# Performance work log

Measured on AMD Instinct MI355X. Metric: run time of the kernel, lower is better.

## Reference

```python
import jax, jax.numpy as jnp
import numpy as np

B, C, H, W = 8, 3, 1024, 1024
N, D, PS, NB, NH = 512, 256, 16, 8, 4


def _bin_matrix():
    # static radial-binning averaging matrix for a PS x (PS//2+1) rfft2 spectrum
    h, w = PS, PS // 2 + 1
    fy = np.fft.fftfreq(h)
    fx = np.linspace(0.0, 0.5, w)
    r = np.sqrt(fx[None, :] ** 2 + fy[:, None] ** 2)
    max_r = r.max() + 1e-6
    edges = np.linspace(0.0, max_r, NB + 1)
    idx = np.clip(np.searchsorted(edges, r.ravel(), side='right') - 1, 0, NB - 1)
    M = np.zeros((NB, h * w), np.float32)
    M[idx, np.arange(h * w)] = 1.0
    cnt = M.sum(1, keepdims=True)
    return M / np.maximum(cnt, 1.0)

_BIN_M = jnp.asarray(_bin_matrix())


def _ln(x, g, b, eps=1e-5):
    m = x.mean(-1, keepdims=True)
    v = x.var(-1, keepdims=True)
    return g * (x - m) / jnp.sqrt(v + eps) + b


def _gelu(x):
    return jax.nn.gelu(x, approximate=False)


def setup_inputs() -> dict:
    key = jax.random.key(0)
    ks = jax.random.split(key, 16)
    xav = lambda k, o, i: (jax.random.normal(k, (o, i)) / np.sqrt(i)).astype(jnp.float32)
    z = lambda n: jnp.zeros((n,), jnp.float32)
    o1 = lambda n: jnp.ones((n,), jnp.float32)
    FD = 2 * NB
    return {
        'image': jax.random.normal(ks[0], (B, C, H, W), jnp.float32),
        'point_coords': jax.random.uniform(ks[1], (B, N, 2), jnp.float32, 0.0, float(W)),
        'point_labels': jax.random.randint(ks[2], (B, N), 0, 2),
        'pe_w': xav(ks[3], D, D), 'pe_b': z(D),
        'type_emb': (0.02 * jax.random.normal(ks[4], (2, D))).astype(jnp.float32),
        'fbi': (1.0 + 0.1 * jax.random.normal(ks[5], (NB,))).astype(jnp.float32),
        'fe1_w': xav(ks[6], D // 2, FD), 'fe1_b': z(D // 2),
        'feln1_g': o1(D // 2), 'feln1_b': z(D // 2),
        'fe2_w': xav(ks[7], D, D // 2), 'fe2_b': z(D),
        'feln2_g': o1(D), 'feln2_b': z(D),
        'in_w': xav(ks[8], 3 * D, D), 'in_b': z(3 * D),
        'ao_w': xav(ks[9], D, D), 'ao_b': z(D),
        'n1_g': o1(D), 'n1_b': z(D),
        'f1_w': xav(ks[10], 2 * D, D), 'f1_b': z(2 * D),
        'f2_w': xav(ks[11], D, 2 * D), 'f2_b': z(D),
        'n2_g': o1(D), 'n2_b': z(D),
        'op_w': xav(ks[12], D, D), 'op_b': z(D),
    }


def reference(image, point_coords, point_labels, pe_w, pe_b, type_emb, fbi,
              fe1_w, fe1_b, feln1_g, feln1_b, fe2_w, fe2_b, feln2_g, feln2_b,
              in_w, in_b, ao_w, ao_b, n1_g, n1_b, f1_w, f1_b, f2_w, f2_b,
              n2_g, n2_b, op_w, op_b):
    Bv, Cv, Hv, Wv = image.shape
    Nv = point_coords.shape[1]
    # --- sinusoidal positional encoding (SAM style) + linear proj ---
    nc = point_coords / jnp.array([Wv, Hv], jnp.float32)
    dim_t = 10000.0 ** (2.0 * jnp.arange(D // 4, dtype=jnp.float32) / (D // 4))
    ax = (nc[..., 0:1] * (2.0 * np.pi)) / dim_t          # [B,N,D/4]
    ay = (nc[..., 1:2] * (2.0 * np.pi)) / dim_t
    pe = jnp.concatenate([jnp.sin(ax), jnp.cos(ax), jnp.sin(ay), jnp.cos(ay)], -1)
    spatial = pe @ pe_w.T + pe_b + type_emb[point_labels]  # [B,N,D]
    # --- batched per-point patch gather + rfft2 + radial binning ---
    gray = image.mean(1)                                   # [B,H,W]
    pc = jax.lax.stop_gradient(point_coords)               # .long() detaches in torch
    half = PS // 2
    px = jnp.clip(pc[..., 0].astype(jnp.int32), half, Wv - half - 1)
    py = jnp.clip(pc[..., 1].astype(jnp.int32), half, Hv - half - 1)
    off = jnp.arange(PS) - half
    rows = py[..., None] + off                             # [B,N,PS]
    cols = px[..., None] + off
    bidx = jnp.arange(Bv)[:, None, None, None]
    patches = gray[bidx, rows[..., :, None], cols[..., None, :]]  # [B,N,PS,PS]
    fft = jnp.fft.rfft2(patches, norm='ortho')             # [B,N,PS,PS//2+1]
    mag_bins = jnp.abs(fft).reshape(Bv, Nv, -1) @ _BIN_M.T    # [B,N,NB]
    ph_bins = jnp.angle(fft).reshape(Bv, Nv, -1) @ _BIN_M.T
    feat = jnp.concatenate([mag_bins * jax.nn.softmax(fbi), ph_bins], -1)  # [B,N,2*NB]
    # --- freq encoder MLP ---
    h1 = _gelu(_ln(feat @ fe1_w.T + fe1_b, feln1_g, feln1_b))
    freq = _ln(h1 @ fe2_w.T + fe2_b, feln2_g, feln2_b)     # [B,N,D]
    # --- cross-attention fusion (spatial = Q, freq = K/V) ---
    hd = D // NH
    q = (spatial @ in_w[:D].T + in_b[:D]).reshape(Bv, Nv, NH, hd)
    k = (freq @ in_w[D:2 * D].T + in_b[D:2 * D]).reshape(Bv, Nv, NH, hd)
    v = (freq @ in_w[2 * D:].T + in_b[2 * D:]).reshape(Bv, Nv, NH, hd)
    att = jax.nn.softmax(jnp.einsum('bqhd,bkhd->bhqk', q, k) / np.sqrt(hd), -1)
    o = jnp.einsum('bhqk,bkhd->bqhd', att, v).reshape(Bv, Nv, D)
    x = _ln(spatial + (o @ ao_w.T + ao_b), n1_g, n1_b)
    ffn = _gelu(x @ f1_w.T + f1_b) @ f2_w.T + f2_b
    x = _ln(x + ffn, n2_g, n2_b)
    return x @ op_w.T + op_b
```

## Files before the change

### kernel.cpp

```cpp
#include <hip/hip_runtime.h>
#include <math.h>


typedef __attribute__((ext_vector_type(8))) short short8;
typedef __attribute__((ext_vector_type(4))) float floatx4;
typedef unsigned short u16;
typedef unsigned long long u64;

__device__ __forceinline__ float gelu_f(float x) {
  return 0.5f * x * (1.0f + erff(x * 0.70710678118654752f));
}

__device__ __forceinline__ u16 bf16_rn(float x) {
  union { float f; unsigned u; } v; v.f = x;
  unsigned r = v.u + 0x7fffu + ((v.u >> 16) & 1u);
  return (u16)(r >> 16);
}

__device__ __forceinline__ void split_bf16(float x, u16& h, u16& l) {
  h = bf16_rn(x);
  union { unsigned u; float f; } hv; hv.u = ((unsigned)h) << 16;
  l = bf16_rn(x - hv.f);
}

__device__ __forceinline__ float join_bf16(u16 h, u16 l) {
  union { unsigned u; float f; } a, b;
  a.u = ((unsigned)h) << 16;
  b.u = ((unsigned)l) << 16;
  return a.f + b.f;
}

#define W_PE   0
#define W_FE1  65536
#define W_FE2  67584
#define W_IN   100352
#define W_AO   296960
#define W_F1   362496
#define W_F2   493568
#define W_OP   624640


template <int NA, int K>
__device__ __forceinline__ void mm16_swz(
    const u16* Ah, const u16* Al, const int S,
    const u16* __restrict__ Bh, const u16* __restrict__ Bl,
    floatx4* acc)
{
  const int t = threadIdx.x;
  const int w = t >> 6, lane = t & 63;
  const int lm = lane & 15, kg = lane >> 4;
  #pragma unroll
  for (int it = 0; it < K / 32; ++it) {
    const short8 a_h = *(const short8*)&Ah[lm * S + it * 32 + kg * 8];
    const short8 a_l = *(const short8*)&Al[lm * S + it * 32 + kg * 8];
    #pragma unroll
    for (int nj = 0; nj < NA; nj++) {
      const size_t wo = (size_t)(((w * NA + nj) * (K / 32) + it) * 512 + lane * 8);
      const short8 b_h = *(const short8*)&Bh[wo];
      const short8 b_l = *(const short8*)&Bl[wo];
      acc[nj] = __builtin_amdgcn_mfma_f32_16x16x32_bf16(a_h, b_h, acc[nj], 0, 0, 0);
      acc[nj] = __builtin_amdgcn_mfma_f32_16x16x32_bf16(a_h, b_l, acc[nj], 0, 0, 0);
      acc[nj] = __builtin_amdgcn_mfma_f32_16x16x32_bf16(a_l, b_h, acc[nj], 0, 0, 0);
    }
  }
}

template <int NA, int K, int NSETS>
__device__ __forceinline__ void mm16_ks(
    const u16* Ah, const u16* Al, const int S,
    const u16* __restrict__ Bh, const u16* __restrict__ Bl,
    floatx4* acc)
{
  const int t = threadIdx.x;
  const int w = t >> 6, lane = t & 63;
  const int ww = w & 3, set = w >> 2;
  const int lm = lane & 15, kg = lane >> 4;
  constexpr int ITERS = K / (32 * NSETS);
  #pragma unroll
  for (int itl = 0; itl < ITERS; ++itl) {
    const int it = set * ITERS + itl;
    const short8 a_h = *(const short8*)&Ah[lm * S + it * 32 + kg * 8];
    const short8 a_l = *(const short8*)&Al[lm * S + it * 32 + kg * 8];
    #pragma unroll
    for (int nj = 0; nj < NA; nj++) {
      const size_t wo = (size_t)(((ww * NA + nj) * (K / 32) + it) * 512 + lane * 8);
      const short8 b_h = *(const short8*)&Bh[wo];
      const short8 b_l = *(const short8*)&Bl[wo];
      acc[nj] = __builtin_amdgcn_mfma_f32_16x16x32_bf16(a_h, b_h, acc[nj], 0, 0, 0);
      acc[nj] = __builtin_amdgcn_mfma_f32_16x16x32_bf16(a_h, b_l, acc[nj], 0, 0, 0);
      acc[nj] = __builtin_amdgcn_mfma_f32_16x16x32_bf16(a_l, b_h, acc[nj], 0, 0, 0);
    }
  }
}

template <int NA>
__device__ __forceinline__ void reduce_sets(floatx4* acc, float* PART)
{
  const int t = threadIdx.x;
  const int w = t >> 6, lane = t & 63;
  const int ww = w & 3, set = w >> 2;
  const int lm = lane & 15, kg = lane >> 4;
  __syncthreads();
  if (set != 0) {
    #pragma unroll
    for (int nj = 0; nj < NA; nj++) {
      const int col = ww * (NA * 16) + nj * 16 + lm;
      #pragma unroll
      for (int r = 0; r < 4; r++)
        PART[((set - 1) * 16 + kg * 4 + r) * 260 + col] = acc[nj][r];
    }
  }
  __syncthreads();
  if (set == 0) {
    #pragma unroll
    for (int nj = 0; nj < NA; nj++) {
      const int col = ww * (NA * 16) + nj * 16 + lm;
      #pragma unroll
      for (int r = 0; r < 4; r++) {
        const int rr = kg * 4 + r;
        acc[nj][r] += PART[rr * 260 + col] + PART[(16 + rr) * 260 + col]
                    + PART[(32 + rr) * 260 + col];
      }
    }
  }
}

__device__ __forceinline__ void stage16(
    const u16* __restrict__ Gh, const u16* __restrict__ Gl,
    u16* Lh, u16* Ll)
{
  const int t = threadIdx.x;
  #pragma unroll
  for (int i = 0; i < 2; i++) {
    const int s = t + i * 256;
    const int row = s >> 5, c = (s & 31) * 8;
    *(short8*)&Lh[row * 264 + c] = *(const short8*)&Gh[(size_t)row * 256 + c];
    *(short8*)&Ll[row * 264 + c] = *(const short8*)&Gl[(size_t)row * 256 + c];
  }
  __syncthreads();
}

template <int N_, int NA>
__device__ __forceinline__ void ln_rows(const float (&v)[NA][4], float* red1, float* red2,
                                        float (&mean)[4], float (&rstd)[4])
{
  const int t = threadIdx.x;
  const int w = t >> 6;
  const int lane = t & 63;
  const int kg = lane >> 4;
  float s1[4] = {0.f,0.f,0.f,0.f}, s2[4] = {0.f,0.f,0.f,0.f};
  #pragma unroll
  for (int nj = 0; nj < NA; nj++)
    #pragma unroll
    for (int r = 0; r < 4; r++) { s1[r] += v[nj][r]; s2[r] += v[nj][r] * v[nj][r]; }
  #pragma unroll
  for (int r = 0; r < 4; r++) {
    #pragma unroll
    for (int off = 1; off < 16; off <<= 1) {
      s1[r] += __shfl_xor(s1[r], off);
      s2[r] += __shfl_xor(s2[r], off);
    }
  }
  __syncthreads();
  if ((lane & 15) == 0) {
    #pragma unroll
    for (int r = 0; r < 4; r++) {
      red1[w * 16 + kg * 4 + r] = s1[r];
      red2[w * 16 + kg * 4 + r] = s2[r];
    }
  }
  __syncthreads();
  #pragma unroll
  for (int r = 0; r < 4; r++) {
    const int rw = kg * 4 + r;
    const float a = red1[rw] + red1[16 + rw] + red1[32 + rw] + red1[48 + rw];
    const float b = red2[rw] + red2[16 + rw] + red2[32 + rw] + red2[48 + rw];
    mean[r] = a * (1.0f / N_);
    rstd[r] = rsqrtf(b * (1.0f / N_) - mean[r] * mean[r] + 1e-5f);
  }
}

template <int N_, int NA>
__device__ __forceinline__ void ln_rows16(const float (&v)[NA][4], float* red1, float* red2,
                                          float (&mean)[4], float (&rstd)[4])
{
  const int t = threadIdx.x;
  const int w = t >> 6;
  const int lane = t & 63;
  const int ww = w & 3, set = w >> 2;
  const int kg = lane >> 4;
  float s1[4] = {0.f,0.f,0.f,0.f}, s2[4] = {0.f,0.f,0.f,0.f};
  #pragma unroll
  for (int nj = 0; nj < NA; nj++)
    #pragma unroll
    for (int r = 0; r < 4; r++) { s1[r] += v[nj][r]; s2[r] += v[nj][r] * v[nj][r]; }
  #pragma unroll
  for (int r = 0; r < 4; r++) {
    #pragma unroll
    for (int off = 1; off < 16; off <<= 1) {
      s1[r] += __shfl_xor(s1[r], off);
      s2[r] += __shfl_xor(s2[r], off);
    }
  }
  __syncthreads();
  if (set == 0 && (lane & 15) == 0) {
    #pragma unroll
    for (int r = 0; r < 4; r++) {
      red1[ww * 16 + kg * 4 + r] = s1[r];
      red2[ww * 16 + kg * 4 + r] = s2[r];
    }
  }
  __syncthreads();
  if (set == 0) {
    #pragma unroll
    for (int r = 0; r < 4; r++) {
      const int rw = kg * 4 + r;
      const float a = red1[rw] + red1[16 + rw] + red1[32 + rw] + red1[48 + rw];
      const float b = red2[rw] + red2[16 + rw] + red2[32 + rw] + red2[48 + rw];
      mean[r] = a * (1.0f / N_);
      rstd[r] = rsqrtf(b * (1.0f / N_) - mean[r] * mean[r] + 1e-5f);
    }
  }
}

__device__ __forceinline__ void store_swz(
    u16* __restrict__ Wh, u16* __restrict__ Wl, const int segbase,
    const int rel, const int kshift, const float4 v)
{
  const int K = 1 << kshift;
  const int n = rel >> kshift;
  const int k = rel & (K - 1);
  const int off8 = ((n >> 4) * (K >> 5) + (k >> 5)) * 512
                 + (((k >> 3) & 3) * 16 + (n & 15)) * 8 + (k & 7);
  u16 h0,h1,h2,h3,l0,l1,l2,l3;
  split_bf16(v.x,h0,l0); split_bf16(v.y,h1,l1);
  split_bf16(v.z,h2,l2); split_bf16(v.w,h3,l3);
  *(u64*)&Wh[segbase + off8] = (u64)h0 | ((u64)h1<<16) | ((u64)h2<<32) | ((u64)h3<<48);
  *(u64*)&Wl[segbase + off8] = (u64)l0 | ((u64)l1<<16) | ((u64)l2<<32) | ((u64)l3<<48);
}

__global__ __launch_bounds__(64) void k0_prep(
    const float* __restrict__ image, const float* __restrict__ coords,
    const float* __restrict__ fbi,
    const float* __restrict__ pe_w, const float* __restrict__ fe1_w,
    const float* __restrict__ fe2_w, const float* __restrict__ in_w,
    const float* __restrict__ ao_w, const float* __restrict__ f1_w,
    const float* __restrict__ f2_w, const float* __restrict__ op_w,
    u16* __restrict__ Wh, u16* __restrict__ Wl,
    u16* __restrict__ PEh, u16* __restrict__ PEl,
    u16* __restrict__ FEATh, u16* __restrict__ FEATl)
{
  const int blk = blockIdx.x;
  const int lane = threadIdx.x;

  if (blk < 2696) {
    const int idx = (blk * 64 + lane) * 4;
    if (idx < W_FE1) {
      store_swz(Wh, Wl, W_PE, idx - W_PE, 8, *(const float4*)&pe_w[idx - W_PE]);
    } else if (idx < W_FE2) {
      const int rel = idx - W_FE1;
      const float4 v = *(const float4*)&fe1_w[rel];
      u16 h0,h1,h2,h3,l0,l1,l2,l3;
      split_bf16(v.x,h0,l0); split_bf16(v.y,h1,l1);
      split_bf16(v.z,h2,l2); split_bf16(v.w,h3,l3);
      *(u64*)&Wh[idx] = (u64)h0 | ((u64)h1<<16) | ((u64)h2<<32) | ((u64)h3<<48);
      *(u64*)&Wl[idx] = (u64)l0 | ((u64)l1<<16) | ((u64)l2<<32) | ((u64)l3<<48);
    } else if (idx < W_IN) {
      store_swz(Wh, Wl, W_FE2, idx - W_FE2, 7, *(const float4*)&fe2_w[idx - W_FE2]);
    } else if (idx < W_AO) {
      store_swz(Wh, Wl, W_IN, idx - W_IN, 8, *(const float4*)&in_w[idx - W_IN]);
    } else if (idx < W_F1) {
      store_swz(Wh, Wl, W_AO, idx - W_AO, 8, *(const float4*)&ao_w[idx - W_AO]);
    } else if (idx < W_F2) {
      store_swz(Wh, Wl, W_F1, idx - W_F1, 8, *(const float4*)&f1_w[idx - W_F1]);
    } else if (idx < W_OP) {
      store_swz(Wh, Wl, W_F2, idx - W_F2, 9, *(const float4*)&f2_w[idx - W_F2]);
    } else {
      store_swz(Wh, Wl, W_OP, idx - W_OP, 8, *(const float4*)&op_w[idx - W_OP]);
    }
    return;
  }

  const int id = blk - 2696;
  const int b  = id >> 9;
  const float pcx = coords[id * 2 + 0];
  const float pcy = coords[id * 2 + 1];

  {
    const float TWO_PI = 6.283185307179586f;
    const float dimt = expf((float)lane * 0.28782313662425572f);
    const float ax = (pcx * (1.0f / 1024.0f)) * TWO_PI / dimt;
    const float ay = (pcy * (1.0f / 1024.0f)) * TWO_PI / dimt;
    u16 h, l;
    split_bf16(sinf(ax), h, l); PEh[id*256+lane]     = h; PEl[id*256+lane]     = l;
    split_bf16(cosf(ax), h, l); PEh[id*256+lane+64]  = h; PEl[id*256+lane+64]  = l;
    split_bf16(sinf(ay), h, l); PEh[id*256+lane+128] = h; PEl[id*256+lane+128] = l;
    split_bf16(cosf(ay), h, l); PEh[id*256+lane+192] = h; PEl[id*256+lane+192] = l;
  }

  int px = (int)pcx; px = px < 8 ? 8 : (px > 1015 ? 1015 : px);
  int py = (int)pcy; py = py < 8 ? 8 : (py > 1015 ? 1015 : py);

  __shared__ float patch[256];
  __shared__ float ct[16], st[16];
  __shared__ float Gre[144], Gim[144];
  __shared__ float msum[8], psum[8];
  __shared__ int cnt8[8];
  {
    const float* img = image + (size_t)b * 3145728;
    #pragma unroll
    for (int i = 0; i < 4; i++) {
      const int p = i * 64 + lane;
      const int r = p >> 4, c = p & 15;
      const int off = (py - 8 + r) * 1024 + (px - 8 + c);
      const float s = img[off] + img[off + 1048576] + img[off + 2097152];
      patch[r * 16 + c] = s * (1.0f / 3.0f);
    }
  }
  if (lane < 16) {
    float c, s;
    if ((lane & 3) == 0) {
      const float cv[4] = {1.0f, 0.0f, -1.0f, 0.0f};
      const float sv[4] = {0.0f, -1.0f, 0.0f, 1.0f};
      c = cv[lane >> 2]; s = sv[lane >> 2];
    } else {
      const float a = -3.14159265358979f * (float)lane * 0.125f;
      c = cosf(a); s = sinf(a);
    }
    ct[lane] = c; st[lane] = s;
  }
  if (lane < 8) { msum[lane] = 0.0f; psum[lane] = 0.0f; cnt8[lane] = 0; }
  __syncthreads();

  for (int tt = lane; tt < 144; tt += 64) {
    const int y = tt / 9, kx = tt - y * 9;
    float re = 0.0f, im = 0.0f;
    #pragma unroll
    for (int x = 0; x < 16; x++) {
      const int w = (x * kx) & 15;
      const float pv = patch[y * 16 + x];
      re = fmaf(pv, ct[w], re);
      im = fmaf(pv, st[w], im);
    }
    Gre[tt] = re; Gim[tt] = im;
  }
  __syncthreads();

  for (int tt = lane; tt < 144; tt += 64) {
    const int ky = tt / 9, kx = tt - ky * 9;
    float re = 0.0f, im = 0.0f;
    #pragma unroll
    for (int y = 0; y < 16; y++) {
      const int w = (y * ky) & 15;
      const float gr = Gre[y * 9 + kx], gi = Gim[y * 9 + kx];
      re = fmaf(gr, ct[w], re);
      re = fmaf(-gi, st[w], re);
      im = fmaf(gr, st[w], im);
      im = fmaf(gi, ct[w], im);
    }
    if (((ky & 7) == 0) && ((kx & 7) == 0)) im = 0.0f;
    const float mag = sqrtf(re * re + im * im) * 0.0625f;
    const float ph  = atan2f(im, re);

    const float fy = (ky < 8) ? (float)ky * 0.0625f : (float)(ky - 16) * 0.0625f;
    const float fx = (float)kx * 0.0625f;
    const float r = sqrtf(fx * fx + fy * fy);
    const float max_r = 0.7071077811865476f;
    const float stepf = max_r * 0.125f;
    int idx = 0;
    #pragma unroll
    for (int kq = 1; kq <= 8; kq++) {
      const float e = (kq == 8) ? max_r : stepf * (float)kq;
      if (r >= e) idx = kq;
    }
    if (idx > 7) idx = 7;
    atomicAdd(&msum[idx], mag);
    atomicAdd(&psum[idx], ph);
    atomicAdd(&cnt8[idx], 1);
  }
  __syncthreads();

  if (lane < 8) {
    float fm = fbi[0];
    #pragma unroll
    for (int j = 1; j < 8; j++) fm = fmaxf(fm, fbi[j]);
    float se = 0.0f;
    #pragma unroll
    for (int j = 0; j < 8; j++) se += expf(fbi[j] - fm);
    const float smx = expf(fbi[lane] - fm) / se;
    const float c = (float)(cnt8[lane] > 0 ? cnt8[lane] : 1);
    u16 h, l;
    split_bf16((msum[lane] / c) * smx, h, l);
    FEATh[id*16+lane] = h; FEATl[id*16+lane] = l;
    split_bf16(psum[lane] / c, h, l);
    FEATh[id*16+8+lane] = h; FEATl[id*16+8+lane] = l;
  }
}

__global__ __launch_bounds__(256) void k1_front(
    const u16* __restrict__ Wh, const u16* __restrict__ Wl,
    const u16* __restrict__ PEh, const u16* __restrict__ PEl,
    const u16* __restrict__ FEATh, const u16* __restrict__ FEATl,
    const float* __restrict__ pe_b, const int* __restrict__ labels,
    const float* __restrict__ temb,
    const float* __restrict__ fe1_b, const float* __restrict__ feln1_g, const float* __restrict__ feln1_b,
    const float* __restrict__ fe2_b, const float* __restrict__ feln2_g, const float* __restrict__ feln2_b,
    const float* __restrict__ in_b,
    u16* __restrict__ SPh, u16* __restrict__ SPl,
    u16* __restrict__ Qh, u16* __restrict__ Ql,
    u16* __restrict__ Kh, u16* __restrict__ Kl,
    u16* __restrict__ Vth, u16* __restrict__ Vtl)
{
  __shared__ __align__(16) u16 smem[12800];
  __shared__ float redbuf[128];
  const int blk = blockIdx.x;
  const int t = threadIdx.x;
  const int w = t >> 6, lane = t & 63;
  const int lm = lane & 15, kg = lane >> 4;

  if (blk < 256) {
    const int m0 = blk * 16;
    u16* Lh = smem;
    u16* Ll = smem + 4224;
    stage16(PEh + (size_t)m0 * 256, PEl + (size_t)m0 * 256, Lh, Ll);
    floatx4 acc[4];
    #pragma unroll
    for (int j = 0; j < 4; j++) acc[j] = (floatx4){0.f,0.f,0.f,0.f};
    mm16_swz<4, 256>(Lh, Ll, 264, Wh + W_PE, Wl + W_PE, acc);
    __syncthreads();
    #pragma unroll
    for (int nj = 0; nj < 4; nj++) {
      const int col = w * 64 + nj * 16 + lm;
      #pragma unroll
      for (int r = 0; r < 4; r++) {
        const int row = m0 + kg * 4 + r;
        const float v = acc[nj][r] + pe_b[col] + temb[labels[row] * 256 + col];
        u16 h, l; split_bf16(v, h, l);
        SPh[(size_t)row * 256 + col] = h;
        SPl[(size_t)row * 256 + col] = l;
        Lh[(kg * 4 + r) * 264 + col] = h;
        Ll[(kg * 4 + r) * 264 + col] = l;
      }
    }
    __syncthreads();

    floatx4 accq[4];
    #pragma unroll
    for (int j = 0; j < 4; j++) accq[j] = (floatx4){0.f,0.f,0.f,0.f};
    mm16_swz<4, 256>(Lh, Ll, 264, Wh + W_IN, Wl + W_IN, accq);
    #pragma unroll
    for (int nj = 0; nj < 4; nj++) {
      const int col = w * 64 + nj * 16 + lm;
      #pragma unroll
      for (int r = 0; r < 4; r++) {
        const int row = m0 + kg * 4 + r;
        u16 h, l; split_bf16(accq[nj][r] + in_b[col], h, l);
        Qh[(size_t)row * 256 + col] = h;
        Ql[(size_t)row * 256 + col] = l;
      }
    }
    return;
  }

  const int m0 = (blk - 256) * 16;
  u16* h1h = smem;
  u16* h1l = smem + 2176;
  u16* Ah  = smem + 4352;
  u16* Al  = smem + 8576;

  floatx4 acc1[2];
  acc1[0] = (floatx4){0.f,0.f,0.f,0.f};
  acc1[1] = (floatx4){0.f,0.f,0.f,0.f};
  {
    const short8 zz = {0,0,0,0,0,0,0,0};
    const short8 a_h = (kg < 2) ? *(const short8*)&FEATh[(size_t)(m0 + lm) * 16 + kg * 8] : zz;
    const short8 a_l = (kg < 2) ? *(const short8*)&FEATl[(size_t)(m0 + lm) * 16 + kg * 8] : zz;
    #pragma unroll
    for (int nj = 0; nj < 2; nj++) {
      const int col = w * 32 + nj * 16 + lm;
      const short8 b_h = (kg < 2) ? *(const short8*)&Wh[W_FE1 + (size_t)col * 16 + kg * 8] : zz;
      const short8 b_l = (kg < 2) ? *(const short8*)&Wl[W_FE1 + (size_t)col * 16 + kg * 8] : zz;
      acc1[nj] = __builtin_amdgcn_mfma_f32_16x16x32_bf16(a_h, b_h, acc1[nj], 0, 0, 0);
      acc1[nj] = __builtin_amdgcn_mfma_f32_16x16x32_bf16(a_h, b_l, acc1[nj], 0, 0, 0);
      acc1[nj] = __builtin_amdgcn_mfma_f32_16x16x32_bf16(a_l, b_h, acc1[nj], 0, 0, 0);
    }
  }

  float v1[2][4];
  #pragma unroll
  for (int nj = 0; nj < 2; nj++) {
    const int col = w * 32 + nj * 16 + lm;
    #pragma unroll
    for (int r = 0; r < 4; r++) v1[nj][r] = acc1[nj][r] + fe1_b[col];
  }
  float mean[4], rstd[4];
  ln_rows<128, 2>(v1, redbuf, redbuf + 64, mean, rstd);
  #pragma unroll
  for (int nj = 0; nj < 2; nj++) {
    const int col = w * 32 + nj * 16 + lm;
    #pragma unroll
    for (int r = 0; r < 4; r++) {
      float y = feln1_g[col] * (v1[nj][r] - mean[r]) * rstd[r] + feln1_b[col];
      y = gelu_f(y);
      u16 h, l; split_bf16(y, h, l);
      h1h[(kg * 4 + r) * 136 + col] = h;
      h1l[(kg * 4 + r) * 136 + col] = l;
    }
  }
  __syncthreads();

  floatx4 acc2[4];
  #pragma unroll
  for (int j = 0; j < 4; j++) acc2[j] = (floatx4){0.f,0.f,0.f,0.f};
  mm16_swz<4, 128>(h1h, h1l, 136, Wh + W_FE2, Wl + W_FE2, acc2);

  float v2[4][4];
  #pragma unroll
  for (int nj = 0; nj < 4; nj++) {
    const int col = w * 64 + nj * 16 + lm;
    #pragma unroll
    for (int r = 0; r < 4; r++) v2[nj][r] = acc2[nj][r] + fe2_b[col];
  }
  ln_rows<256, 4>(v2, redbuf, redbuf + 64, mean, rstd);
  #pragma unroll
  for (int nj = 0; nj < 4; nj++) {
    const int col = w * 64 + nj * 16 + lm;
    #pragma unroll
    for (int r = 0; r < 4; r++) {
      float y = feln2_g[col] * (v2[nj][r] - mean[r]) * rstd[r] + feln2_b[col];
      u16 h, l; split_bf16(y, h, l);
      Ah[(kg * 4 + r) * 264 + col] = h;
      Al[(kg * 4 + r) * 264 + col] = l;
    }
  }
  __syncthreads();

  {
    floatx4 acck[4];
    #pragma unroll
    for (int j = 0; j < 4; j++) acck[j] = (floatx4){0.f,0.f,0.f,0.f};
    mm16_swz<4, 256>(Ah, Al, 264, Wh + W_IN + 65536, Wl + W_IN + 65536, acck);
    #pragma unroll
    for (int nj = 0; nj < 4; nj++) {
      const int col = w * 64 + nj * 16 + lm;
      #pragma unroll
      for (int r = 0; r < 4; r++) {
        const int row = m0 + kg * 4 + r;
        u16 h, l; split_bf16(acck[nj][r] + in_b[256 + col], h, l);
        Kh[(size_t)row * 256 + col] = h;
        Kl[(size_t)row * 256 + col] = l;
      }
    }
  }

  {
    floatx4 accv[4];
    #pragma unroll
    for (int j = 0; j < 4; j++) accv[j] = (floatx4){0.f,0.f,0.f,0.f};
    mm16_swz<4, 256>(Ah, Al, 264, Wh + W_IN + 131072, Wl + W_IN + 131072, accv);
    #pragma unroll
    for (int nj = 0; nj < 4; nj++) {
      const int col = w * 64 + nj * 16 + lm;
      u64 hp = 0, lp = 0;
      #pragma unroll
      for (int r = 0; r < 4; r++) {
        u16 h, l; split_bf16(accv[nj][r] + in_b[512 + col], h, l);
        hp |= ((u64)h) << (16 * r);
        lp |= ((u64)l) << (16 * r);
      }
      *(u64*)&Vth[(size_t)col * 4096 + m0 + kg * 4] = hp;
      *(u64*)&Vtl[(size_t)col * 4096 + m0 + kg * 4] = lp;
    }
  }
}

__global__ __launch_bounds__(512) void k3_attn(
    const u16* __restrict__ Qh, const u16* __restrict__ Ql,
    const u16* __restrict__ Kh, const u16* __restrict__ Kl,
    const u16* __restrict__ Vth, const u16* __restrict__ Vtl,
    u16* __restrict__ Oh, u16* __restrict__ Ol)
{
  __shared__ __align__(16) u16 smem[64512];
  __shared__ float O1[64 * 68];
  __shared__ float Mbuf[64], Lbuf[64];

  const int t = threadIdx.x;
  const int w = t >> 6, lane = t & 63;
  const int ww = w & 3, set = w >> 2;
  const int lm = lane & 15, kg = lane >> 4;
  const int ts = t & 255;

  u16* sQh = smem;
  u16* sQl = smem + 4608;
  u16* sKh = smem + 9216 + set * 27648;
  u16* sKl = sKh + 4608;
  u16* sVh = sKh + 9216;
  u16* sVl = sKh + 13824;
  u16* sPh = sKh + 18432;
  u16* sPl = sKh + 23040;

  const int qt = blockIdx.x & 7;
  const int bh = blockIdx.x >> 3;
  const int b = bh >> 2, h = bh & 3;
  const int qrow0 = b * 512 + qt * 64;

  {
    const int r = t >> 3, d = (t & 7) * 8;
    *(short8*)&sQh[r * 72 + d] = *(const short8*)&Qh[(size_t)(qrow0 + r) * 256 + h * 64 + d];
    *(short8*)&sQl[r * 72 + d] = *(const short8*)&Ql[(size_t)(qrow0 + r) * 256 + h * 64 + d];
  }

  float m_i[4], l_i[4];
  floatx4 o_acc[4];
  #pragma unroll
  for (int r = 0; r < 4; r++) { m_i[r] = -INFINITY; l_i[r] = 0.0f; }
  #pragma unroll
  for (int dj = 0; dj < 4; dj++) o_acc[dj] = (floatx4){0.f, 0.f, 0.f, 0.f};

  __syncthreads();
  short8 q_h[2], q_l[2];
  #pragma unroll
  for (int ks = 0; ks < 2; ks++) {
    const int off = (ww * 16 + lm) * 72 + ks * 32 + kg * 8;
    q_h[ks] = *(const short8*)&sQh[off];
    q_l[ks] = *(const short8*)&sQl[off];
  }

  for (int ktl = 0; ktl < 4; ktl++) {
    const int kt = set * 4 + ktl;
    __syncthreads();
    {
      const int krow0 = b * 512 + kt * 64;
      #pragma unroll
      for (int i = 0; i < 2; i++) {
        const int s = ts + i * 256;
        const int r = s >> 3, d = (s & 7) * 8;
        *(short8*)&sKh[r * 72 + d] = *(const short8*)&Kh[(size_t)(krow0 + r) * 256 + h * 64 + d];
        *(short8*)&sKl[r * 72 + d] = *(const short8*)&Kl[(size_t)(krow0 + r) * 256 + h * 64 + d];
        *(short8*)&sVh[r * 72 + d] = *(const short8*)&Vth[(size_t)(h * 64 + r) * 4096 + krow0 + d];
        *(short8*)&sVl[r * 72 + d] = *(const short8*)&Vtl[(size_t)(h * 64 + r) * 4096 + krow0 + d];
      }
    }
    __syncthreads();

    floatx4 sacc[4];
    #pragma unroll
    for (int nj = 0; nj < 4; nj++) sacc[nj] = (floatx4){0.f, 0.f, 0.f, 0.f};
    #pragma unroll
    for (int ks = 0; ks < 2; ks++) {
      #pragma unroll
      for (int nj = 0; nj < 4; nj++) {
        const int off = (nj * 16 + lm) * 72 + ks * 32 + kg * 8;
        const short8 kb_h = *(const short8*)&sKh[off];
        const short8 kb_l = *(const short8*)&sKl[off];
        sacc[nj] = __builtin_amdgcn_mfma_f32_16x16x32_bf16(q_h[ks], kb_h, sacc[nj], 0, 0, 0);
        sacc[nj] = __builtin_amdgcn_mfma_f32_16x16x32_bf16(q_h[ks], kb_l, sacc[nj], 0, 0, 0);
        sacc[nj] = __builtin_amdgcn_mfma_f32_16x16x32_bf16(q_l[ks], kb_h, sacc[nj], 0, 0, 0);
      }
    }

    float pp[4][4];
    #pragma unroll
    for (int r = 0; r < 4; r++) {
      float mx = -INFINITY;
      #pragma unroll
      for (int nj = 0; nj < 4; nj++) {
        sacc[nj][r] *= 0.125f;
        mx = fmaxf(mx, sacc[nj][r]);
      }
      #pragma unroll
      for (int off = 1; off < 16; off <<= 1) mx = fmaxf(mx, __shfl_xor(mx, off));
      const float mnew = fmaxf(m_i[r], mx);
      const float alpha = expf(m_i[r] - mnew);
      m_i[r] = mnew;
      float rs = 0.0f;
      #pragma unroll
      for (int nj = 0; nj < 4; nj++) { pp[nj][r] = expf(sacc[nj][r] - mnew); rs += pp[nj][r]; }
      #pragma unroll
      for (int off = 1; off < 16; off <<= 1) rs += __shfl_xor(rs, off);
      l_i[r] = l_i[r] * alpha + rs;
      #pragma unroll
      for (int dj = 0; dj < 4; dj++) o_acc[dj][r] *= alpha;
    }

    #pragma unroll
    for (int nj = 0; nj < 4; nj++)
      #pragma unroll
      for (int r = 0; r < 4; r++) {
        u16 ph, pl; split_bf16(pp[nj][r], ph, pl);
        sPh[(ww * 16 + kg * 4 + r) * 72 + nj * 16 + lm] = ph;
        sPl[(ww * 16 + kg * 4 + r) * 72 + nj * 16 + lm] = pl;
      }

    #pragma unroll
    for (int ks = 0; ks < 2; ks++) {
      const short8 p_h = *(const short8*)&sPh[(ww * 16 + lm) * 72 + ks * 32 + kg * 8];
      const short8 p_l = *(const short8*)&sPl[(ww * 16 + lm) * 72 + ks * 32 + kg * 8];
      #pragma unroll
      for (int dj = 0; dj < 4; dj++) {
        const int off = (dj * 16 + lm) * 72 + ks * 32 + kg * 8;
        const short8 v_h = *(const short8*)&sVh[off];
        const short8 v_l = *(const short8*)&sVl[off];
        o_acc[dj] = __builtin_amdgcn_mfma_f32_16x16x32_bf16(p_h, v_h, o_acc[dj], 0, 0, 0);
        o_acc[dj] = __builtin_amdgcn_mfma_f32_16x16x32_bf16(p_l, v_h, o_acc[dj], 0, 0, 0);
        o_acc[dj] = __builtin_amdgcn_mfma_f32_16x16x32_bf16(p_h, v_l, o_acc[dj], 0, 0, 0);
      }
    }
  }

  if (set == 1) {
    #pragma unroll
    for (int r = 0; r < 4; r++) {
      const int row = ww * 16 + kg * 4 + r;
      if (lm == 0) { Mbuf[row] = m_i[r]; Lbuf[row] = l_i[r]; }
      #pragma unroll
      for (int dj = 0; dj < 4; dj++)
        O1[row * 68 + dj * 16 + lm] = o_acc[dj][r];
    }
  }
  __syncthreads();
  if (set == 0) {
    #pragma unroll
    for (int r = 0; r < 4; r++) {
      const int row = ww * 16 + kg * 4 + r;
      const float m1 = Mbuf[row], l1v = Lbuf[row];
      const float mnew = fmaxf(m_i[r], m1);
      const float a0 = expf(m_i[r] - mnew);
      const float a1 = expf(m1 - mnew);
      const float inv_l = 1.0f / (l_i[r] * a0 + l1v * a1);
      const size_t rowoff = (size_t)(qrow0 + row) * 256 + h * 64;
      #pragma unroll
      for (int dj = 0; dj < 4; dj++) {
        const float val = (o_acc[dj][r] * a0 + O1[row * 68 + dj * 16 + lm] * a1) * inv_l;
        u16 hh, ll; split_bf16(val, hh, ll);
        Oh[rowoff + dj * 16 + lm] = hh;
        Ol[rowoff + dj * 16 + lm] = ll;
      }
    }
  }
}

__global__ __launch_bounds__(1024) void k4_tail(
    const u16* __restrict__ Wh, const u16* __restrict__ Wl,
    const u16* __restrict__ Oh, const u16* __restrict__ Ol,
    const u16* __restrict__ SPh, const u16* __restrict__ SPl,
    const float* __restrict__ ao_b, const float* __restrict__ n1_g, const float* __restrict__ n1_b,
    const float* __restrict__ f1_b, const float* __restrict__ f2_b,
    const float* __restrict__ n2_g, const float* __restrict__ n2_b,
    const float* __restrict__ op_b, float* __restrict__ OUT)
{
  __shared__ __align__(16) u16 smem[25088];
  __shared__ float redbuf[128];
  __shared__ float PART[3 * 16 * 260];
  u16* B1h = smem;
  u16* B1l = smem + 4224;
  u16* Fh  = smem + 8448;
  u16* Fl  = smem + 16768;

  const int t = threadIdx.x;
  const int w = t >> 6, lane = t & 63;
  const int ww = w & 3, set = w >> 2;
  const int lm = lane & 15, kg = lane >> 4;
  const int m0 = blockIdx.x * 16;

  {
    const u16* Gh = Oh + (size_t)m0 * 256;
    const u16* Gl = Ol + (size_t)m0 * 256;
    if (t < 512) {
      const int row = t >> 5, c = (t & 31) * 8;
      *(short8*)&B1h[row * 264 + c] = *(const short8*)&Gh[(size_t)row * 256 + c];
      *(short8*)&B1l[row * 264 + c] = *(const short8*)&Gl[(size_t)row * 256 + c];
    }
    __syncthreads();
  }

  floatx4 acc[4];
  #pragma unroll
  for (int j = 0; j < 4; j++) acc[j] = (floatx4){0.f,0.f,0.f,0.f};
  mm16_ks<4, 256, 4>(B1h, B1l, 264, Wh + W_AO, Wl + W_AO, acc);
  reduce_sets<4>(acc, PART);

  float x1reg[4][4];
  {
    float v[4][4];
    if (set == 0) {
      #pragma unroll
      for (int nj = 0; nj < 4; nj++) {
        const int col = ww * 64 + nj * 16 + lm;
        #pragma unroll
        for (int r = 0; r < 4; r++) {
          const size_t si = (size_t)(m0 + kg * 4 + r) * 256 + col;
          v[nj][r] = acc[nj][r] + ao_b[col] + join_bf16(SPh[si], SPl[si]);
        }
      }
    } else {
      #pragma unroll
      for (int nj = 0; nj < 4; nj++)
        #pragma unroll
        for (int r = 0; r < 4; r++) v[nj][r] = 0.0f;
    }
    float mean[4], rstd[4];
    ln_rows16<256, 4>(v, redbuf, redbuf + 64, mean, rstd);
    if (set == 0) {
      #pragma unroll
      for (int nj = 0; nj < 4; nj++) {
        const int col = ww * 64 + nj * 16 + lm;
        #pragma unroll
        for (int r = 0; r < 4; r++) {
          const float y = n1_g[col] * (v[nj][r] - mean[r]) * rstd[r] + n1_b[col];
          x1reg[nj][r] = y;
          u16 h, l; split_bf16(y, h, l);
          B1h[(kg * 4 + r) * 264 + col] = h;
          B1l[(kg * 4 + r) * 264 + col] = l;
        }
      }
    }
  }
  __syncthreads();

  #pragma unroll
  for (int ct = 0; ct < 2; ct++) {
    floatx4 a4[4];
    #pragma unroll
    for (int j = 0; j < 4; j++) a4[j] = (floatx4){0.f,0.f,0.f,0.f};
    mm16_ks<4, 256, 4>(B1h, B1l, 264,
                       Wh + W_F1 + (size_t)ct * 65536, Wl + W_F1 + (size_t)ct * 65536, a4);
    reduce_sets<4>(a4, PART);
    if (set == 0) {
      #pragma unroll
      for (int nj = 0; nj < 4; nj++) {
        const int col = ct * 256 + ww * 64 + nj * 16 + lm;
        #pragma unroll
        for (int r = 0; r < 4; r++) {
          const float y = gelu_f(a4[nj][r] + f1_b[col]);
          u16 h, l; split_bf16(y, h, l);
          Fh[(kg * 4 + r) * 520 + col] = h;
          Fl[(kg * 4 + r) * 520 + col] = l;
        }
      }
    }
  }
  __syncthreads();

  #pragma unroll
  for (int j = 0; j < 4; j++) acc[j] = (floatx4){0.f,0.f,0.f,0.f};
  mm16_ks<4, 512, 4>(Fh, Fl, 520, Wh + W_F2, Wl + W_F2, acc);
  reduce_sets<4>(acc, PART);
  {
    float v[4][4];
    if (set == 0) {
      #pragma unroll
      for (int nj = 0; nj < 4; nj++) {
        const int col = ww * 64 + nj * 16 + lm;
        #pragma unroll
        for (int r = 0; r < 4; r++)
          v[nj][r] = acc[nj][r] + f2_b[col] + x1reg[nj][r];
      }
    } else {
      #pragma unroll
      for (int nj = 0; nj < 4; nj++)
        #pragma unroll
        for (int r = 0; r < 4; r++) v[nj][r] = 0.0f;
    }
    float mean[4], rstd[4];
    ln_rows16<256, 4>(v, redbuf, redbuf + 64, mean, rstd);
    if (set == 0) {
      #pragma unroll
      for (int nj = 0; nj < 4; nj++) {
        const int col = ww * 64 + nj * 16 + lm;
        #pragma unroll
        for (int r = 0; r < 4; r++) {
          const float y = n2_g[col] * (v[nj][r] - mean[r]) * rstd[r] + n2_b[col];
          u16 h, l; split_bf16(y, h, l);
          B1h[(kg * 4 + r) * 264 + col] = h;
          B1l[(kg * 4 + r) * 264 + col] = l;
        }
      }
    }
  }
  __syncthreads();

  #pragma unroll
  for (int j = 0; j < 4; j++) acc[j] = (floatx4){0.f,0.f,0.f,0.f};
  mm16_ks<4, 256, 4>(B1h, B1l, 264, Wh + W_OP, Wl + W_OP, acc);
  reduce_sets<4>(acc, PART);
  if (set == 0) {
    #pragma unroll
    for (int nj = 0; nj < 4; nj++) {
      const int col = ww * 64 + nj * 16 + lm;
      #pragma unroll
      for (int r = 0; r < 4; r++)
        OUT[(size_t)(m0 + kg * 4 + r) * 256 + col] = acc[nj][r] + op_b[col];
    }
  }
}

extern "C" void kernel_launch(void* const* d_in, const int* in_sizes, int n_in,
                              void* d_out, int out_size, void* d_ws, size_t ws_size,
                              hipStream_t stream) {
  const float* image   = (const float*)d_in[0];
  const float* coords  = (const float*)d_in[1];
  const int*   labels  = (const int*)d_in[2];
  const float* pe_w    = (const float*)d_in[3];
  const float* pe_b    = (const float*)d_in[4];
  const float* temb    = (const float*)d_in[5];
  const float* fbi     = (const float*)d_in[6];
  const float* fe1_w   = (const float*)d_in[7];
  const float* fe1_b   = (const float*)d_in[8];
  const float* feln1_g = (const float*)d_in[9];
  const float* feln1_b = (const float*)d_in[10];
  const float* fe2_w   = (const float*)d_in[11];
  const float* fe2_b   = (const float*)d_in[12];
  const float* feln2_g = (const float*)d_in[13];
  const float* feln2_b = (const float*)d_in[14];
  const float* in_w    = (const float*)d_in[15];
  const float* in_b    = (const float*)d_in[16];
  const float* ao_w    = (const float*)d_in[17];
  const float* ao_b    = (const float*)d_in[18];
  const float* n1_g    = (const float*)d_in[19];
  const float* n1_b    = (const float*)d_in[20];
  const float* f1_w    = (const float*)d_in[21];
  const float* f1_b    = (const float*)d_in[22];
  const float* f2_w    = (const float*)d_in[23];
  const float* f2_b    = (const float*)d_in[24];
  const float* n2_g    = (const float*)d_in[25];
  const float* n2_b    = (const float*)d_in[26];
  const float* op_w    = (const float*)d_in[27];
  const float* op_b    = (const float*)d_in[28];

  float* ws = (float*)d_ws;
  u16* S = (u16*)(ws + 2 * (1u << 20));
  u16* Wh = S;
  u16* Wl = S + 690176;
  u16* PEh   = S + 1380352;  u16* PEl   = PEh + 1048576;
  u16* FEATh = S + 3477504;  u16* FEATl = FEATh + 65536;
  u16* SPh   = S + 6754304;  u16* SPl   = SPh + 1048576;
  u16* Qh    = S + 8851456;  u16* Ql    = Qh + 1048576;
  u16* Kh    = S + 10948608; u16* Kl    = Kh + 1048576;
  u16* Vth   = S + 13045760; u16* Vtl   = Vth + 1048576;
  u16* Oh    = S + 15142912; u16* Ol    = Oh + 1048576;

  float* OUT = (float*)d_out;

  k0_prep<<<6792, 64, 0, stream>>>(
      image, coords, fbi, pe_w, fe1_w, fe2_w, in_w, ao_w, f1_w, f2_w, op_w,
      Wh, Wl, PEh, PEl, FEATh, FEATl);
  k1_front<<<512, 256, 0, stream>>>(
      Wh, Wl, PEh, PEl, FEATh, FEATl, pe_b, labels, temb,
      fe1_b, feln1_g, feln1_b, fe2_b, feln2_g, feln2_b, in_b,
      SPh, SPl, Qh, Ql, Kh, Kl, Vth, Vtl);
  k3_attn<<<256, 512, 0, stream>>>(Qh, Ql, Kh, Kl, Vth, Vtl, Oh, Ol);
  k4_tail<<<256, 1024, 0, stream>>>(
      Wh, Wl, Oh, Ol, SPh, SPl, ao_b, n1_g, n1_b, f1_b, f2_b, n2_g, n2_b, op_b, OUT);
}
```

Measured before the change: 289.0 us.

## Fuse attention kernel into tail kernel with per-wave split-K softmax merge

New measurement: 298.5 us. 1.03x slower.

```diff
diff --git a/kernel.cpp b/kernel.cpp
--- a/kernel.cpp
+++ b/kernel.cpp
@@ -574,205 +574,174 @@
   }
 }
 
-__global__ __launch_bounds__(512) void k3_attn(
+__global__ __launch_bounds__(1024) void k34_attn_tail(
+    const u16* __restrict__ Wh, const u16* __restrict__ Wl,
     const u16* __restrict__ Qh, const u16* __restrict__ Ql,
     const u16* __restrict__ Kh, const u16* __restrict__ Kl,
     const u16* __restrict__ Vth, const u16* __restrict__ Vtl,
-    u16* __restrict__ Oh, u16* __restrict__ Ol)
-{
-  __shared__ __align__(16) u16 smem[64512];
-  __shared__ float O1[64 * 68];
-  __shared__ float Mbuf[64], Lbuf[64];
-
-  const int t = threadIdx.x;
-  const int w = t >> 6, lane = t & 63;
-  const int ww = w & 3, set = w >> 2;
-  const int lm = lane & 15, kg = lane >> 4;
-  const int ts = t & 255;
-
-  u16* sQh = smem;
-  u16* sQl = smem + 4608;
-  u16* sKh = smem + 9216 + set * 27648;
-  u16* sKl = sKh + 4608;
-  u16* sVh = sKh + 9216;
-  u16* sVl = sKh + 13824;
-  u16* sPh = sKh + 18432;
-  u16* sPl = sKh + 23040;
-
-  const int qt = blockIdx.x & 7;
-  const int bh = blockIdx.x >> 3;
-  const int b = bh >> 2, h = bh & 3;
-  const int qrow0 = b * 512 + qt * 64;
-
-  {
-    const int r = t >> 3, d = (t & 7) * 8;
-    *(short8*)&sQh[r * 72 + d] = *(const short8*)&Qh[(size_t)(qrow0 + r) * 256 + h * 64 + d];
-    *(short8*)&sQl[r * 72 + d] = *(const short8*)&Ql[(size_t)(qrow0 + r) * 256 + h * 64 + d];
-  }
-
-  float m_i[4], l_i[4];
-  floatx4 o_acc[4];
-  #pragma unroll
-  for (int r = 0; r < 4; r++) { m_i[r] = -INFINITY; l_i[r] = 0.0f; }
-  #pragma unroll
-  for (int dj = 0; dj < 4; dj++) o_acc[dj] = (floatx4){0.f, 0.f, 0.f, 0.f};
-
-  __syncthreads();
-  short8 q_h[2], q_l[2];
-  #pragma unroll
-  for (int ks = 0; ks < 2; ks++) {
-    const int off = (ww * 16 + lm) * 72 + ks * 32 + kg * 8;
-    q_h[ks] = *(const short8*)&sQh[off];
-    q_l[ks] = *(const short8*)&sQl[off];
-  }
-
-  for (int ktl = 0; ktl < 4; ktl++) {
-    const int kt = set * 4 + ktl;
-    __syncthreads();
-    {
-      const int krow0 = b * 512 + kt * 64;
-      #pragma unroll
-      for (int i = 0; i < 2; i++) {
-        const int s = ts + i * 256;
-        const int r = s >> 3, d = (s & 7) * 8;
-        *(short8*)&sKh[r * 72 + d] = *(const short8*)&Kh[(size_t)(krow0 + r) * 256 + h * 64 + d];
-        *(short8*)&sKl[r * 72 + d] = *(const short8*)&Kl[(size_t)(krow0 + r) * 256 + h * 64 + d];
-        *(short8*)&sVh[r * 72 + d] = *(const short8*)&Vth[(size_t)(h * 64 + r) * 4096 + krow0 + d];
-        *(short8*)&sVl[r * 72 + d] = *(const short8*)&Vtl[(size_t)(h * 64 + r) * 4096 + krow0 + d];
-      }
-    }
-    __syncthreads();
-
-    floatx4 sacc[4];
-    #pragma unroll
-    for (int nj = 0; nj < 4; nj++) sacc[nj] = (floatx4){0.f, 0.f, 0.f, 0.f};
-    #pragma unroll
-    for (int ks = 0; ks < 2; ks++) {
-      #pragma unroll
-      for (int nj = 0; nj < 4; nj++) {
-        const int off = (nj * 16 + lm) * 72 + ks * 32 + kg * 8;
-        const short8 kb_h = *(const short8*)&sKh[off];
-        const short8 kb_l = *(const short8*)&sKl[off];
-        sacc[nj] = __builtin_amdgcn_mfma_f32_16x16x32_bf16(q_h[ks], kb_h, sacc[nj], 0, 0, 0);
-        sacc[nj] = __builtin_amdgcn_mfma_f32_16x16x32_bf16(q_h[ks], kb_l, sacc[nj], 0, 0, 0);
-        sacc[nj] = __builtin_amdgcn_mfma_f32_16x16x32_bf16(q_l[ks], kb_h, sacc[nj], 0, 0, 0);
-      }
-    }
-
-    float pp[4][4];
-    #pragma unroll
-    for (int r = 0; r < 4; r++) {
-      float mx = -INFINITY;
-      #pragma unroll
-      for (int nj = 0; nj < 4; nj++) {
-        sacc[nj][r] *= 0.125f;
-        mx = fmaxf(mx, sacc[nj][r]);
-      }
-      #pragma unroll
-      for (int off = 1; off < 16; off <<= 1) mx = fmaxf(mx, __shfl_xor(mx, off));
-      const float mnew = fmaxf(m_i[r], mx);
-      const float alpha = expf(m_i[r] - mnew);
-      m_i[r] = mnew;
-      float rs = 0.0f;
-      #pragma unroll
-      for (int nj = 0; nj < 4; nj++) { pp[nj][r] = expf(sacc[nj][r] - mnew); rs += pp[nj][r]; }
-      #pragma unroll
-      for (int off = 1; off < 16; off <<= 1) rs += __shfl_xor(rs, off);
-      l_i[r] = l_i[r] * alpha + rs;
-      #pragma unroll
-      for (int dj = 0; dj < 4; dj++) o_acc[dj][r] *= alpha;
-    }
-
-    #pragma unroll
-    for (int nj = 0; nj < 4; nj++)
-      #pragma unroll
-      for (int r = 0; r < 4; r++) {
-        u16 ph, pl; split_bf16(pp[nj][r], ph, pl);
-        sPh[(ww * 16 + kg * 4 + r) * 72 + nj * 16 + lm] = ph;
-        sPl[(ww * 16 + kg * 4 + r) * 72 + nj * 16 + lm] = pl;
-      }
-
-    #pragma unroll
-    for (int ks = 0; ks < 2; ks++) {
-      const short8 p_h = *(const short8*)&sPh[(ww * 16 + lm) * 72 + ks * 32 + kg * 8];
-      const short8 p_l = *(const short8*)&sPl[(ww * 16 + lm) * 72 + ks * 32 + kg * 8];
-      #pragma unroll
-      for (int dj = 0; dj < 4; dj++) {
-        const int off = (dj * 16 + lm) * 72 + ks * 32 + kg * 8;
-        const short8 v_h = *(const short8*)&sVh[off];
-        const short8 v_l = *(const short8*)&sVl[off];
-        o_acc[dj] = __builtin_amdgcn_mfma_f32_16x16x32_bf16(p_h, v_h, o_acc[dj], 0, 0, 0);
-        o_acc[dj] = __builtin_amdgcn_mfma_f32_16x16x32_bf16(p_l, v_h, o_acc[dj], 0, 0, 0);
-        o_acc[dj] = __builtin_amdgcn_mfma_f32_16x16x32_bf16(p_h, v_l, o_acc[dj], 0, 0, 0);
-      }
-    }
-  }
-
-  if (set == 1) {
-    #pragma unroll
-    for (int r = 0; r < 4; r++) {
-      const int row = ww * 16 + kg * 4 + r;
-      if (lm == 0) { Mbuf[row] = m_i[r]; Lbuf[row] = l_i[r]; }
-      #pragma unroll
-      for (int dj = 0; dj < 4; dj++)
-        O1[row * 68 + dj * 16 + lm] = o_acc[dj][r];
-    }
-  }
-  __syncthreads();
-  if (set == 0) {
-    #pragma unroll
-    for (int r = 0; r < 4; r++) {
-      const int row = ww * 16 + kg * 4 + r;
-      const float m1 = Mbuf[row], l1v = Lbuf[row];
-      const float mnew = fmaxf(m_i[r], m1);
-      const float a0 = expf(m_i[r] - mnew);
-      const float a1 = expf(m1 - mnew);
-      const float inv_l = 1.0f / (l_i[r] * a0 + l1v * a1);
-      const size_t rowoff = (size_t)(qrow0 + row) * 256 + h * 64;
-      #pragma unroll
-      for (int dj = 0; dj < 4; dj++) {
-        const float val = (o_acc[dj][r] * a0 + O1[row * 68 + dj * 16 + lm] * a1) * inv_l;
-        u16 hh, ll; split_bf16(val, hh, ll);
-        Oh[rowoff + dj * 16 + lm] = hh;
-        Ol[rowoff + dj * 16 + lm] = ll;
-      }
-    }
-  }
-}
-
-__global__ __launch_bounds__(1024) void k4_tail(
-    const u16* __restrict__ Wh, const u16* __restrict__ Wl,
-    const u16* __restrict__ Oh, const u16* __restrict__ Ol,
     const u16* __restrict__ SPh, const u16* __restrict__ SPl,
     const float* __restrict__ ao_b, const float* __restrict__ n1_g, const float* __restrict__ n1_b,
     const float* __restrict__ f1_b, const float* __restrict__ f2_b,
     const float* __restrict__ n2_g, const float* __restrict__ n2_b,
     const float* __restrict__ op_b, float* __restrict__ OUT)
 {
-  __shared__ __align__(16) u16 smem[25088];
+  __shared__ __align__(16) u16 smem[8448 + 41600];
   __shared__ float redbuf[128];
-  __shared__ float PART[3 * 16 * 260];
+  __shared__ float MLs[16 * 16 * 2];
   u16* B1h = smem;
   u16* B1l = smem + 4224;
-  u16* Fh  = smem + 8448;
-  u16* Fl  = smem + 16768;
+  u16* pool = smem + 8448;
 
   const int t = threadIdx.x;
   const int w = t >> 6, lane = t & 63;
-  const int ww = w & 3, set = w >> 2;
   const int lm = lane & 15, kg = lane >> 4;
   const int m0 = blockIdx.x * 16;
-
-  {
-    const u16* Gh = Oh + (size_t)m0 * 256;
-    const u16* Gl = Ol + (size_t)m0 * 256;
-    if (t < 512) {
-      const int row = t >> 5, c = (t & 31) * 8;
-      *(short8*)&B1h[row * 264 + c] = *(const short8*)&Gh[(size_t)row * 256 + c];
-      *(short8*)&B1l[row * 264 + c] = *(const short8*)&Gl[(size_t)row * 256 + c];
-    }
-    __syncthreads();
-  }
+  const int b = m0 >> 9;
+  const int h = w & 3, g = w >> 2;
+
+  u16* sPh = pool + w * 2304;
+  u16* sPl = sPh + 1152;
+
+  short8 q_h[2], q_l[2];
+  #pragma unroll
+  for (int ks = 0; ks < 2; ks++) {
+    const size_t qo = (size_t)(m0 + lm) * 256 + h * 64 + ks * 32 + kg * 8;
+    q_h[ks] = *(const short8*)&Qh[qo];
+    q_l[ks] = *(const short8*)&Ql[qo];
+  }
+
+  float m_i[4], l_i[4];
+  floatx4 o_acc[4];
+  #pragma unroll
+  for (int r = 0; r < 4; r++) { m_i[r] = -INFINITY; l_i[r] = 0.0f; }
+  #pragma unroll
+  for (int dj = 0; dj < 4; dj++) o_acc[dj] = (floatx4){0.f, 0.f, 0.f, 0.f};
+
+  for (int kti = 0; kti < 2; kti++) {
+    const int kt = g * 2 + kti;
+    const int krow0 = b * 512 + kt * 64;
+
+    floatx4 sacc[4];
+    #pragma unroll
+    for (int nj = 0; nj < 4; nj++) sacc[nj] = (floatx4){0.f, 0.f, 0.f, 0.f};
+    #pragma unroll
+    for (int ks = 0; ks < 2; ks++) {
+      #pragma unroll
+      for (int nj = 0; nj < 4; nj++) {
+        const size_t ko = (size_t)(krow0 + nj * 16 + lm) * 256 + h * 64 + ks * 32 + kg * 8;
+        const short8 kb_h = *(const short8*)&Kh[ko];
+        const short8 kb_l = *(const short8*)&Kl[ko];
+        sacc[nj] = __builtin_amdgcn_mfma_f32_16x16x32_bf16(q_h[ks], kb_h, sacc[nj], 0, 0, 0);
+        sacc[nj] = __builtin_amdgcn_mfma_f32_16x16x32_bf16(q_h[ks], kb_l, sacc[nj], 0, 0, 0);
+        sacc[nj] = __builtin_amdgcn_mfma_f32_16x16x32_bf16(q_l[ks], kb_h, sacc[nj], 0, 0, 0);
+      }
+    }
+
+    float pp[4][4];
+    #pragma unroll
+    for (int r = 0; r < 4; r++) {
+      float mx = -INFINITY;
+      #pragma unroll
+      for (int nj = 0; nj < 4; nj++) {
+        sacc[nj][r] *= 0.125f;
+        mx = fmaxf(mx, sacc[nj][r]);
+      }
+      #pragma unroll
+      for (int off = 1; off < 16; off <<= 1) mx = fmaxf(mx, __shfl_xor(mx, off));
+      const float mnew = fmaxf(m_i[r], mx);
+      const float alpha = expf(m_i[r] - mnew);
+      m_i[r] = mnew;
+      float rs = 0.0f;
+      #pragma unroll
+      for (int nj = 0; nj < 4; nj++) { pp[nj][r] = expf(sacc[nj][r] - mnew); rs += pp[nj][r]; }
+      #pragma unroll
+      for (int off = 1; off < 16; off <<= 1) rs += __shfl_xor(rs, off);
+      l_i[r] = l_i[r] * alpha + rs;
+      #pragma unroll
+      for (int dj = 0; dj < 4; dj++) o_acc[dj][r] *= alpha;
+    }
+
+    #pragma unroll
+    for (int nj = 0; nj < 4; nj++)
+      #pragma unroll
+      for (int r = 0; r < 4; r++) {
+        u16 ph, pl; split_bf16(pp[nj][r], ph, pl);
+        sPh[(kg * 4 + r) * 72 + nj * 16 + lm] = ph;
+        sPl[(kg * 4 + r) * 72 + nj * 16 + lm] = pl;
+      }
+
+    #pragma unroll
+    for (int ks = 0; ks < 2; ks++) {
+      const short8 p_h = *(const short8*)&sPh[lm * 72 + ks * 32 + kg * 8];
+      const short8 p_l = *(const short8*)&sPl[lm * 72 + ks * 32 + kg * 8];
+      #pragma unroll
+      for (int dj = 0; dj < 4; dj++) {
+        const size_t vo = (size_t)(h * 64 + dj * 16 + lm) * 4096 + krow0 + ks * 32 + kg * 8;
+        const short8 v_h = *(const short8*)&Vth[vo];
+        const short8 v_l = *(const short8*)&Vtl[vo];
+        o_acc[dj] = __builtin_amdgcn_mfma_f32_16x16x32_bf16(p_h, v_h, o_acc[dj], 0, 0, 0);
+        o_acc[dj] = __builtin_amdgcn_mfma_f32_16x16x32_bf16(p_l, v_h, o_acc[dj], 0, 0, 0);
+        o_acc[dj] = __builtin_amdgcn_mfma_f32_16x16x32_bf16(p_h, v_l, o_acc[dj], 0, 0, 0);
+      }
+    }
+  }
+
+  __syncthreads();
+
+  float* MRG = (float*)pool;
+  if (lm == 0) {
+    #pragma unroll
+    for (int r = 0; r < 4; r++) {
+      MLs[(w * 16 + kg * 4 + r) * 2]     = m_i[r];
+      MLs[(w * 16 + kg * 4 + r) * 2 + 1] = l_i[r];
+    }
+  }
+  if (g != 0) {
+    float* dst = MRG + ((g - 1) * 4 + h) * 1024;
+    #pragma unroll
+    for (int dj = 0; dj < 4; dj++)
+      #pragma unroll
+      for (int r = 0; r < 4; r++)
+        dst[(kg * 4 + r) * 64 + dj * 16 + lm] = o_acc[dj][r];
+  }
+  __syncthreads();
+  if (g == 0) {
+    #pragma unroll
+    for (int r = 0; r < 4; r++) {
+      const int row = kg * 4 + r;
+      float mstar = m_i[r];
+      float mm[3], ll[3];
+      #pragma unroll
+      for (int gg = 1; gg < 4; gg++) {
+        mm[gg - 1] = MLs[((gg * 4 + h) * 16 + row) * 2];
+        ll[gg - 1] = MLs[((gg * 4 + h) * 16 + row) * 2 + 1];
+        mstar = fmaxf(mstar, mm[gg - 1]);
+      }
+      const float a0 = expf(m_i[r] - mstar);
+      float ag[3];
+      float lstar = l_i[r] * a0;
+      #pragma unroll
+      for (int gg = 0; gg < 3; gg++) { ag[gg] = expf(mm[gg] - mstar); lstar += ll[gg] * ag[gg]; }
+      const float inv = 1.0f / lstar;
+      #pragma unroll
+      for (int dj = 0; dj < 4; dj++) {
+        float val = o_acc[dj][r] * a0;
+        #pragma unroll
+        for (int gg = 0; gg < 3; gg++)
+          val += MRG[(gg * 4 + h) * 1024 + row * 64 + dj * 16 + lm] * ag[gg];
+        val *= inv;
+        u16 hh, llv; split_bf16(val, hh, llv);
+        B1h[row * 264 + h * 64 + dj * 16 + lm] = hh;
+        B1l[row * 264 + h * 64 + dj * 16 + lm] = llv;
+      }
+    }
+  }
+  __syncthreads();
+
+  u16* Fh = pool;
+  u16* Fl = pool + 8320;
+  float* PART = (float*)(pool + 16640);
+  const int ww = w & 3, set = w >> 2;
 
   floatx4 acc[4];
   #pragma unroll
@@ -809,9 +778,9 @@
         for (int r = 0; r < 4; r++) {
           const float y = n1_g[col] * (v[nj][r] - mean[r]) * rstd[r] + n1_b[col];
           x1reg[nj][r] = y;
-          u16 h, l; split_bf16(y, h, l);
-          B1h[(kg * 4 + r) * 264 + col] = h;
-          B1l[(kg * 4 + r) * 264 + col] = l;
+          u16 hh, ll; split_bf16(y, hh, ll);
+          B1h[(kg * 4 + r) * 264 + col] = hh;
+          B1l[(kg * 4 + r) * 264 + col] = ll;
         }
       }
     }
@@ -833,9 +802,9 @@
         #pragma unroll
         for (int r = 0; r < 4; r++) {
           const float y = gelu_f(a4[nj][r] + f1_b[col]);
-          u16 h, l; split_bf16(y, h, l);
-          Fh[(kg * 4 + r) * 520 + col] = h;
-          Fl[(kg * 4 + r) * 520 + col] = l;
+          u16 hh, ll; split_bf16(y, hh, ll);
+          Fh[(kg * 4 + r) * 520 + col] = hh;
+          Fl[(kg * 4 + r) * 520 + col] = ll;
         }
       }
     }
@@ -871,9 +840,9 @@
         #pragma unroll
         for (int r = 0; r < 4; r++) {
           const float y = n2_g[col] * (v[nj][r] - mean[r]) * rstd[r] + n2_b[col];
-          u16 h, l; split_bf16(y, h, l);
-          B1h[(kg * 4 + r) * 264 + col] = h;
-          B1l[(kg * 4 + r) * 264 + col] = l;
+          u16 hh, ll; split_bf16(y, hh, ll);
+          B1h[(kg * 4 + r) * 264 + col] = hh;
+          B1l[(kg * 4 + r) * 264 + col] = ll;
         }
       }
     }
@@ -938,7 +907,6 @@
   u16* Qh    = S + 8851456;  u16* Ql    = Qh + 1048576;
   u16* Kh    = S + 10948608; u16* Kl    = Kh + 1048576;
   u16* Vth   = S + 13045760; u16* Vtl   = Vth + 1048576;
-  u16* Oh    = S + 15142912; u16* Ol    = Oh + 1048576;
 
   float* OUT = (float*)d_out;
 
@@ -949,7 +917,7 @@
       Wh, Wl, PEh, PEl, FEATh, FEATl, pe_b, labels, temb,
       fe1_b, feln1_g, feln1_b, fe2_b, feln2_g, feln2_b, in_b,
       SPh, SPl, Qh, Ql, Kh, Kl, Vth, Vtl);
-  k3_attn<<<256, 512, 0, stream>>>(Qh, Ql, Kh, Kl, Vth, Vtl, Oh, Ol);
-  k4_tail<<<256, 1024, 0, stream>>>(
-      Wh, Wl, Oh, Ol, SPh, SPl, ao_b, n1_g, n1_b, f1_b, f2_b, n2_g, n2_b, op_b, OUT);
-}
+  k34_attn_tail<<<256, 1024, 0, stream>>>(
+      Wh, Wl, Qh, Ql, Kh, Kl, Vth, Vtl, SPh, SPl,
+      ao_b, n1_g, n1_b, f1_b, f2_b, n2_g, n2_b, op_b, OUT);
+}
```
